# Performance work log

Hardware: AMD Instinct MI355X
Metric: run time of the kernel (lower is better)

Reference implementation:

```python
import jax, jax.numpy as jnp
import numpy as np

HEADS = 16
D_MODEL = 1024
D_K = D_MODEL // HEADS
BATCH = 4
SEQ = 1024
NEG_BIG = -1000000000.0


def setup_inputs() -> dict:
    key = jax.random.key(0)
    ks = jax.random.split(key, 7)
    s = 1.0 / np.sqrt(D_MODEL)
    return {
        "q": jax.random.normal(ks[0], (BATCH, SEQ, D_MODEL), jnp.float32),
        "k": jax.random.normal(ks[1], (BATCH, SEQ, D_MODEL), jnp.float32),
        "v": jax.random.normal(ks[2], (BATCH, SEQ, D_MODEL), jnp.float32),
        "Wq": jax.random.normal(ks[3], (D_MODEL, D_MODEL), jnp.float32) * s,
        "Wk": jax.random.normal(ks[4], (D_MODEL, D_MODEL), jnp.float32) * s,
        "Wv": jax.random.normal(ks[5], (D_MODEL, D_MODEL), jnp.float32) * s,
        "Wo": jax.random.normal(ks[6], (D_MODEL, D_MODEL), jnp.float32) * s,
    }


def reference(q, k, v, Wq, Wk, Wv, Wo):
    bs = q.shape[0]
    residual = q
    # torch Linear(bias=False): x @ W.T ; then the module's quirky reshape
    # view(bs, h, -1, d_k) on the contiguous [bs, seq, d_model] buffer.
    qh = (q @ Wq.T).reshape(bs, HEADS, -1, D_K)   # [b, h, s, d_k]
    kh = (k @ Wk.T).reshape(bs, HEADS, -1, D_K)
    vh = (v @ Wv.T).reshape(bs, HEADS, -1, D_K)
    scores = jnp.einsum("bhqd,bhkd->bhqk", qh, kh) / jnp.sqrt(
        jnp.asarray(D_K, qh.dtype))
    # data-dependent mask: exact-zero scores get -1e9 before softmax
    scores = jnp.where(scores == 0, jnp.asarray(NEG_BIG, scores.dtype), scores)
    attn = jax.nn.softmax(scores, axis=-1)  # dropout is identity in eval mode
    out = jnp.einsum("bhqk,bhkd->bhqd", attn, vh)  # [b, h, s, d_k]
    concat = jnp.swapaxes(out, 1, 2).reshape(bs, -1, D_MODEL)
    return concat @ Wo.T + residual
```

## Files before the change

### kernel.cpp

```cpp
#include <hip/hip_runtime.h>
#include <stdint.h>

typedef __bf16 bf16x8 __attribute__((ext_vector_type(8)));
typedef __bf16 bf16x2v __attribute__((ext_vector_type(2)));
typedef float f32x4 __attribute__((ext_vector_type(4)));
typedef uint16_t u16x8 __attribute__((ext_vector_type(8)));
typedef uint16_t u16x4 __attribute__((ext_vector_type(4)));

#define DMODEL 1024
#define K1SC 0.1803368801111244f

__device__ __forceinline__ uint16_t bfc(float f) {
  __bf16 h = (__bf16)f;
  return __builtin_bit_cast(uint16_t, h);
}
__device__ __forceinline__ uint32_t pk32(float a, float b) {
  bf16x2v t = {(__bf16)a, (__bf16)b};
  return __builtin_bit_cast(uint32_t, t);
}
__device__ __forceinline__ void gld16(const void* src, void* dst) {
  __builtin_amdgcn_global_load_lds((const __attribute__((address_space(1))) void*)src,
                                   (__attribute__((address_space(3))) void*)dst, 16, 0, 0);
}

__global__ void cvt_all_kernel(const float* __restrict__ q, const float* __restrict__ k,
                               const float* __restrict__ v, const float* __restrict__ Wq,
                               const float* __restrict__ Wk, const float* __restrict__ Wv,
                               const float* __restrict__ Wo, uint16_t* __restrict__ qb,
                               uint16_t* __restrict__ kb, uint16_t* __restrict__ vb,
                               uint16_t* __restrict__ Wqb, uint16_t* __restrict__ Wkb,
                               uint16_t* __restrict__ Wvb, uint16_t* __restrict__ Wob) {
  int bid = blockIdx.x;
  const float* src;
  uint16_t* dst;
  int off;
  if (bid < 12288) {
    int s = bid >> 12;
    src = s == 0 ? q : (s == 1 ? k : v);
    dst = s == 0 ? qb : (s == 1 ? kb : vb);
    off = bid & 4095;
  } else {
    int r = bid - 12288;
    int s = r >> 10;
    src = s == 0 ? Wq : (s == 1 ? Wk : (s == 2 ? Wv : Wo));
    dst = s == 0 ? Wqb : (s == 1 ? Wkb : (s == 2 ? Wvb : Wob));
    off = r & 1023;
  }
  int i = off * 256 + threadIdx.x;
  f32x4 x = ((const f32x4*)src)[i];
  u16x4 r;
#pragma unroll
  for (int j = 0; j < 4; ++j) r[j] = bfc(x[j]);
  ((u16x4*)dst)[i] = r;
}

__global__ __launch_bounds__(256, 2)
void gemm_qkv_kernel(const uint16_t* __restrict__ A0, const uint16_t* __restrict__ A1,
                     const uint16_t* __restrict__ A2, const uint16_t* __restrict__ W0,
                     const uint16_t* __restrict__ W1, const uint16_t* __restrict__ W2,
                     uint16_t* __restrict__ C0, uint16_t* __restrict__ C1,
                     uint16_t* __restrict__ C2) {
  int orig = blockIdx.x;
  int lin = (orig & 7) * 96 + (orig >> 3);
  int z = lin >> 8;
  int rem = lin & 255;
  int m0 = (rem >> 3) * 128, n0 = (rem & 7) * 128;

  const uint16_t* A = z == 0 ? A0 : (z == 1 ? A1 : A2);
  const uint16_t* Bw = z == 0 ? W0 : (z == 1 ? W1 : W2);
  uint16_t* C = z == 0 ? C0 : (z == 1 ? C1 : C2);
  const float osc = (z == 0) ? K1SC : 1.0f;

  __shared__ __align__(16) uint16_t As[2][128 * 32];
  __shared__ __align__(16) uint16_t Bs[2][128 * 32];
  const int t = threadIdx.x;
  const int lane = t & 63;
  const int w = t >> 6;
  const int wr = w >> 1, wc = w & 1;
  const int lr = lane & 15, ksl = lane >> 4;
  const int sw2 = (lr & 3) << 4;

  f32x4 acc[4][4];
#pragma unroll
  for (int m = 0; m < 4; ++m)
#pragma unroll
    for (int n = 0; n < 4; ++n) acc[m][n] = (f32x4){0.f, 0.f, 0.f, 0.f};

  auto stage = [&](int buf, int k0) {
#pragma unroll
    for (int cc = 0; cc < 2; ++cc) {
      int idx = cc * 256 + t;
      int row = idx >> 2, ch = idx & 3;
      int so = ((ch * 16) ^ ((row & 3) << 4)) >> 1;
      gld16(A + (size_t)(m0 + row) * DMODEL + k0 + so, &As[buf][idx * 8]);
    }
#pragma unroll
    for (int cc = 0; cc < 2; ++cc) {
      int idx = cc * 256 + t;
      int row = idx >> 2, ch = idx & 3;
      int so = ((ch * 16) ^ ((row & 3) << 4)) >> 1;
      gld16(Bw + (size_t)(n0 + row) * DMODEL + k0 + so, &Bs[buf][idx * 8]);
    }
  };

  stage(0, 0);
  __syncthreads();

  int cur = 0;
#pragma unroll 1
  for (int kt = 0; kt < 32; ++kt) {
    if (kt < 31) stage(cur ^ 1, (kt + 1) * 32);
    const char* Ab = (const char*)&As[cur][0];
    const char* Bb = (const char*)&Bs[cur][0];
    const int co = (ksl * 16) ^ sw2;
    bf16x8 af[4], bfv[4];
#pragma unroll
    for (int m = 0; m < 4; ++m)
      af[m] = *(const bf16x8*)(Ab + (wr * 64 + m * 16 + lr) * 64 + co);
#pragma unroll
    for (int n = 0; n < 4; ++n)
      bfv[n] = *(const bf16x8*)(Bb + (wc * 64 + n * 16 + lr) * 64 + co);
    __builtin_amdgcn_s_setprio(1);
#pragma unroll
    for (int m = 0; m < 4; ++m)
#pragma unroll
      for (int n = 0; n < 4; ++n)
        acc[m][n] = __builtin_amdgcn_mfma_f32_16x16x32_bf16(af[m], bfv[n], acc[m][n], 0, 0, 0);
    __builtin_amdgcn_s_setprio(0);
    __syncthreads();
    cur ^= 1;
  }

#pragma unroll
  for (int m = 0; m < 4; ++m) {
#pragma unroll
    for (int n = 0; n < 4; ++n) {
      int col = n0 + wc * 64 + n * 16 + lr;
#pragma unroll
      for (int r = 0; r < 4; ++r) {
        int row = m0 + wr * 64 + m * 16 + ksl * 4 + r;
        C[(size_t)row * DMODEL + col] = bfc(acc[m][n][r] * osc);
      }
    }
  }
}

__global__ __launch_bounds__(256, 2)
void gemm_o_kernel(const uint16_t* __restrict__ A, const uint16_t* __restrict__ Bw,
                   float* __restrict__ Cf, const float* __restrict__ resid) {
  int orig = blockIdx.x;
  int lin = (orig & 7) * 64 + (orig >> 3);
  int m0 = (lin >> 3) * 64, n0 = (lin & 7) * 128;

  __shared__ __align__(16) uint16_t As[2][64 * 32];
  __shared__ __align__(16) uint16_t Bs[2][128 * 32];
  const int t = threadIdx.x;
  const int lane = t & 63;
  const int w = t >> 6;
  const int wr = w >> 1, wc = w & 1;
  const int lr = lane & 15, ksl = lane >> 4;
  const int sw2 = (lr & 3) << 4;

  f32x4 acc[2][4];
#pragma unroll
  for (int m = 0; m < 2; ++m)
#pragma unroll
    for (int n = 0; n < 4; ++n) acc[m][n] = (f32x4){0.f, 0.f, 0.f, 0.f};

  auto stage = [&](int buf, int k0) {
    {
      int row = t >> 2, ch = t & 3;
      int so = ((ch * 16) ^ ((row & 3) << 4)) >> 1;
      gld16(A + (size_t)(m0 + row) * DMODEL + k0 + so, &As[buf][t * 8]);
    }
#pragma unroll
    for (int cc = 0; cc < 2; ++cc) {
      int idx = cc * 256 + t;
      int row = idx >> 2, ch = idx & 3;
      int so = ((ch * 16) ^ ((row & 3) << 4)) >> 1;
      gld16(Bw + (size_t)(n0 + row) * DMODEL + k0 + so, &Bs[buf][idx * 8]);
    }
  };

  stage(0, 0);
  __syncthreads();

  int cur = 0;
#pragma unroll 1
  for (int kt = 0; kt < 32; ++kt) {
    if (kt < 31) stage(cur ^ 1, (kt + 1) * 32);
    const char* Ab = (const char*)&As[cur][0];
    const char* Bb = (const char*)&Bs[cur][0];
    const int co = (ksl * 16) ^ sw2;
    bf16x8 af[2], bfv[4];
#pragma unroll
    for (int m = 0; m < 2; ++m)
      af[m] = *(const bf16x8*)(Ab + (wr * 32 + m * 16 + lr) * 64 + co);
#pragma unroll
    for (int n = 0; n < 4; ++n)
      bfv[n] = *(const bf16x8*)(Bb + (wc * 64 + n * 16 + lr) * 64 + co);
    __builtin_amdgcn_s_setprio(1);
#pragma unroll
    for (int m = 0; m < 2; ++m)
#pragma unroll
      for (int n = 0; n < 4; ++n)
        acc[m][n] = __builtin_amdgcn_mfma_f32_16x16x32_bf16(af[m], bfv[n], acc[m][n], 0, 0, 0);
    __builtin_amdgcn_s_setprio(0);
    __syncthreads();
    cur ^= 1;
  }

#pragma unroll
  for (int m = 0; m < 2; ++m) {
#pragma unroll
    for (int n = 0; n < 4; ++n) {
      int col = n0 + wc * 64 + n * 16 + lr;
#pragma unroll
      for (int r = 0; r < 4; ++r) {
        int row = m0 + wr * 32 + m * 16 + ksl * 4 + r;
        size_t idx = (size_t)row * DMODEL + col;
        Cf[idx] = acc[m][n][r] + resid[idx];
      }
    }
  }
}

__global__ __launch_bounds__(256, 2)
void attn_mfma_kernel(const uint16_t* __restrict__ Pq, const uint16_t* __restrict__ Pk,
                      const uint16_t* __restrict__ Pv, uint16_t* __restrict__ Cc) {
  __shared__ __align__(16) uint16_t Ks[2][64 * 64];
  __shared__ __align__(16) uint16_t Vts[2][64 * 64];
  __shared__ __align__(16) uint16_t Ps[4][16 * 64];

  const int t = threadIdx.x;
  const int w = t >> 6;
  const int lane = t & 63;
  const int lr = lane & 15;
  const int ksl = lane >> 4;
  int orig = blockIdx.x;
  int lin = (orig & 7) * 128 + (orig >> 3);
  const int bh = lin >> 4, qt = lin & 15;
  const int b = bh >> 4, h = bh & 15;

  const uint16_t* Qb = Pq + (size_t)bh * 65536 + (size_t)qt * 64 * 64;
  const uint16_t* Kb = Pk + (size_t)bh * 65536;
  const uint16_t* Vb = Pv + (size_t)bh * 65536;

  bf16x8 qf[2];
  {
    const uint16_t* qrow = Qb + (size_t)(w * 16 + lr) * 64 + ksl * 8;
    qf[0] = *(const bf16x8*)(qrow);
    qf[1] = *(const bf16x8*)(qrow + 32);
  }

  f32x4 Oa[4];
#pragma unroll
  for (int n = 0; n < 4; ++n) Oa[n] = (f32x4){0.f, 0.f, 0.f, 0.f};
  f32x4 lsum4 = {0.f, 0.f, 0.f, 0.f};

  const int p2 = t & 31;
  const int c8 = t >> 5;
  const int sw = (lr & 7) << 4;
  u16x8 va, vb2;

  auto stageK = [&](int buf, int kt) {
#pragma unroll
    for (int cc = 0; cc < 2; ++cc) {
      int idx = cc * 256 + t;
      int row = idx >> 3;
      int bo = (idx & 7) * 16;
      int srcb = bo ^ ((row & 7) << 4);
      gld16(Kb + (size_t)(kt * 64 + row) * 64 + (srcb >> 1), &Ks[buf][idx * 8]);
    }
  };
  auto loadV = [&](int kt) {
    const uint16_t* s0 = Vb + (size_t)(kt * 64 + p2 * 2) * 64 + c8 * 8;
    va = *(const u16x8*)s0;
    vb2 = *(const u16x8*)(s0 + 64);
  };
  auto writeV = [&](int buf) {
    char* base = (char*)&Vts[buf][0];
#pragma unroll
    for (int i = 0; i < 8; ++i) {
      int d = c8 * 8 + i;
      uint32_t val = (uint32_t)va[i] | ((uint32_t)vb2[i] << 16);
      *(uint32_t*)(base + d * 128 + ((p2 * 4) ^ ((d & 7) << 4))) = val;
    }
  };

  stageK(0, 0);
  loadV(0);
  writeV(0);
  __syncthreads();

  int cur = 0;
#pragma unroll 1
  for (int kt = 0; kt < 16; ++kt) {
    if (kt < 15) { stageK(cur ^ 1, kt + 1); loadV(kt + 1); }

    f32x4 S[4];
#pragma unroll
    for (int n = 0; n < 4; ++n) S[n] = (f32x4){0.f, 0.f, 0.f, 0.f};
    __builtin_amdgcn_s_setprio(1);
#pragma unroll
    for (int n = 0; n < 4; ++n) {
      const char* kbp = (const char*)&Ks[cur][0] + (n * 16 + lr) * 128;
#pragma unroll
      for (int c = 0; c < 2; ++c) {
        bf16x8 kf = *(const bf16x8*)(kbp + ((c * 64 + ksl * 16) ^ sw));
        S[n] = __builtin_amdgcn_mfma_f32_16x16x32_bf16(kf, qf[c], S[n], 0, 0, 0);
      }
    }
    __builtin_amdgcn_s_setprio(0);

    f32x4 psum = {0.f, 0.f, 0.f, 0.f};
    f32x4 p4[4];
#pragma unroll
    for (int n = 0; n < 4; ++n) {
#pragma unroll
      for (int r = 0; r < 4; ++r) {
        float x = S[n][r];
        float e = __builtin_amdgcn_exp2f(x);
        p4[n][r] = (x == 0.f) ? 0.f : e;
      }
      psum += p4[n];
    }
    lsum4 += psum;

    char* pb = (char*)&Ps[w][0] + lr * 128;
#pragma unroll
    for (int n = 0; n < 4; ++n) {
      int co = (n * 16 + ksl * 4) * 2;
      *(uint32_t*)(pb + (co ^ sw)) = pk32(p4[n][0], p4[n][1]);
      *(uint32_t*)(pb + ((co + 4) ^ sw)) = pk32(p4[n][2], p4[n][3]);
    }

    __builtin_amdgcn_s_setprio(1);
#pragma unroll
    for (int c = 0; c < 2; ++c) {
      bf16x8 pf = *(const bf16x8*)(pb + ((c * 64 + ksl * 16) ^ sw));
#pragma unroll
      for (int n = 0; n < 4; ++n) {
        const char* vbp = (const char*)&Vts[cur][0] + (n * 16 + lr) * 128;
        bf16x8 vf = *(const bf16x8*)(vbp + ((c * 64 + ksl * 16) ^ sw));
        Oa[n] = __builtin_amdgcn_mfma_f32_16x16x32_bf16(pf, vf, Oa[n], 0, 0, 0);
      }
    }
    __builtin_amdgcn_s_setprio(0);

    if (kt < 15) writeV(cur ^ 1);
    __syncthreads();
    cur ^= 1;
  }

  float lrow = (lsum4[0] + lsum4[1]) + (lsum4[2] + lsum4[3]);
  lrow += __shfl_xor(lrow, 16);
  lrow += __shfl_xor(lrow, 32);
  f32x4 inv4;
#pragma unroll
  for (int r = 0; r < 4; ++r) inv4[r] = 1.f / __shfl(lrow, ksl * 4 + r);

  uint16_t* dst = Cc + (size_t)b * 1048576 + (size_t)(qt * 64 + w * 16) * 1024 + h * 64;
#pragma unroll
  for (int r = 0; r < 4; ++r) {
    int qq = ksl * 4 + r;
#pragma unroll
    for (int n = 0; n < 4; ++n) {
      dst[qq * 1024 + n * 16 + lr] = bfc(Oa[n][r] * inv4[r]);
    }
  }
}

extern "C" void kernel_launch(void* const* d_in, const int* in_sizes, int n_in,
                              void* d_out, int out_size, void* d_ws, size_t ws_size,
                              hipStream_t stream) {
  const float* q  = (const float*)d_in[0];
  const float* k  = (const float*)d_in[1];
  const float* v  = (const float*)d_in[2];
  const float* Wq = (const float*)d_in[3];
  const float* Wk = (const float*)d_in[4];
  const float* Wv = (const float*)d_in[5];
  const float* Wo = (const float*)d_in[6];
  float* out = (float*)d_out;
  char* ws = (char*)d_ws;
  const size_t MB = 1u << 20;
  uint16_t* qb  = (uint16_t*)(ws + 0 * MB);
  uint16_t* kb  = (uint16_t*)(ws + 8 * MB);
  uint16_t* vb  = (uint16_t*)(ws + 16 * MB);
  uint16_t* Wqb = (uint16_t*)(ws + 24 * MB);
  uint16_t* Wkb = (uint16_t*)(ws + 26 * MB);
  uint16_t* Wvb = (uint16_t*)(ws + 28 * MB);
  uint16_t* Wob = (uint16_t*)(ws + 30 * MB);
  uint16_t* Pq  = (uint16_t*)(ws + 32 * MB);
  uint16_t* Pk  = (uint16_t*)(ws + 40 * MB);
  uint16_t* Pv  = (uint16_t*)(ws + 48 * MB);
  uint16_t* Cc  = (uint16_t*)(ws + 56 * MB);

  cvt_all_kernel<<<16384, 256, 0, stream>>>(q, k, v, Wq, Wk, Wv, Wo,
                                            qb, kb, vb, Wqb, Wkb, Wvb, Wob);

  gemm_qkv_kernel<<<768, 256, 0, stream>>>(qb, kb, vb, Wqb, Wkb, Wvb,
                                           Pq, Pk, Pv);

  attn_mfma_kernel<<<1024, 256, 0, stream>>>(Pq, Pk, Pv, Cc);

  gemm_o_kernel<<<512, 256, 0, stream>>>(Cc, Wob, out, q);
}
```

Baseline: 107.1 us.

## Pre-transpose V and feed P directly from registers via 16x16x16 MFMA

Adds a separate kernel that transposes the V projection per head into a d-major buffer, reusing the qb workspace, so the attention kernel can stage V with async global-to-LDS loads instead of register loads and scattered LDS writes. When the 16x16x16 bf16 MFMA builtin is available, P is taken straight from the score accumulators as the A operand, which removes the per-wave P round trip through LDS. Occupancy hint raised to 4 blocks per SM. Costs an extra kernel launch and an additional V read/write through global memory.

```diff
diff --git a/kernel.cpp b/kernel.cpp
--- a/kernel.cpp
+++ b/kernel.cpp
@@ -6,9 +6,17 @@
 typedef float f32x4 __attribute__((ext_vector_type(4)));
 typedef uint16_t u16x8 __attribute__((ext_vector_type(8)));
 typedef uint16_t u16x4 __attribute__((ext_vector_type(4)));
+typedef uint32_t u32x2 __attribute__((ext_vector_type(2)));
+typedef short s16x4 __attribute__((ext_vector_type(4)));
 
 #define DMODEL 1024
 #define K1SC 0.1803368801111244f
+
+#if __has_builtin(__builtin_amdgcn_mfma_f32_16x16x16bf16_1k)
+#define HAS_MFMA16 1
+#else
+#define HAS_MFMA16 0
+#endif
 
 __device__ __forceinline__ uint16_t bfc(float f) {
   __bf16 h = (__bf16)f;
@@ -145,6 +153,32 @@
   }
 }
 
+__global__ void transposeV_kernel(const uint16_t* __restrict__ Pv,
+                                  uint16_t* __restrict__ Vt) {
+  __shared__ uint16_t Ts[64 * 65];
+  const int bh = blockIdx.x >> 4, kt = blockIdx.x & 15;
+  const uint16_t* src = Pv + (size_t)bh * 65536 + (size_t)kt * 64 * 64;
+  uint16_t* dst = Vt + (size_t)bh * 65536 + kt * 64;
+  const int t = threadIdx.x;
+#pragma unroll
+  for (int p = 0; p < 2; ++p) {
+    int idx = p * 256 + t;
+    int kr = idx >> 3, c8 = (idx & 7) * 8;
+    u16x8 ld = *(const u16x8*)(src + kr * 64 + c8);
+#pragma unroll
+    for (int i = 0; i < 8; ++i) Ts[kr * 65 + c8 + i] = ld[i];
+  }
+  __syncthreads();
+  const int dk = t >> 2, jg = t & 3;
+  u16x8 o0, o1;
+#pragma unroll
+  for (int jj = 0; jj < 8; ++jj) o0[jj] = Ts[(jg * 16 + jj) * 65 + dk];
+#pragma unroll
+  for (int jj = 0; jj < 8; ++jj) o1[jj] = Ts[(jg * 16 + 8 + jj) * 65 + dk];
+  *(u16x8*)(dst + (size_t)dk * 1024 + jg * 16) = o0;
+  *(u16x8*)(dst + (size_t)dk * 1024 + jg * 16 + 8) = o1;
+}
+
 __global__ __launch_bounds__(256, 2)
 void gemm_o_kernel(const uint16_t* __restrict__ A, const uint16_t* __restrict__ Bw,
                    float* __restrict__ Cf, const float* __restrict__ resid) {
@@ -225,12 +259,14 @@
   }
 }
 
-__global__ __launch_bounds__(256, 2)
+__global__ __launch_bounds__(256, 4)
 void attn_mfma_kernel(const uint16_t* __restrict__ Pq, const uint16_t* __restrict__ Pk,
-                      const uint16_t* __restrict__ Pv, uint16_t* __restrict__ Cc) {
+                      const uint16_t* __restrict__ Vt, uint16_t* __restrict__ Cc) {
   __shared__ __align__(16) uint16_t Ks[2][64 * 64];
   __shared__ __align__(16) uint16_t Vts[2][64 * 64];
+#if !HAS_MFMA16
   __shared__ __align__(16) uint16_t Ps[4][16 * 64];
+#endif
 
   const int t = threadIdx.x;
   const int w = t >> 6;
@@ -244,7 +280,7 @@
 
   const uint16_t* Qb = Pq + (size_t)bh * 65536 + (size_t)qt * 64 * 64;
   const uint16_t* Kb = Pk + (size_t)bh * 65536;
-  const uint16_t* Vb = Pv + (size_t)bh * 65536;
+  const uint16_t* Vb = Vt + (size_t)bh * 65536;
 
   bf16x8 qf[2];
   {
@@ -258,10 +294,7 @@
   for (int n = 0; n < 4; ++n) Oa[n] = (f32x4){0.f, 0.f, 0.f, 0.f};
   f32x4 lsum4 = {0.f, 0.f, 0.f, 0.f};
 
-  const int p2 = t & 31;
-  const int c8 = t >> 5;
   const int sw = (lr & 7) << 4;
-  u16x8 va, vb2;
 
   auto stageK = [&](int buf, int kt) {
 #pragma unroll
@@ -273,30 +306,25 @@
       gld16(Kb + (size_t)(kt * 64 + row) * 64 + (srcb >> 1), &Ks[buf][idx * 8]);
     }
   };
-  auto loadV = [&](int kt) {
-    const uint16_t* s0 = Vb + (size_t)(kt * 64 + p2 * 2) * 64 + c8 * 8;
-    va = *(const u16x8*)s0;
-    vb2 = *(const u16x8*)(s0 + 64);
+  auto stageV = [&](int buf, int kt) {
+#pragma unroll
+    for (int cc = 0; cc < 2; ++cc) {
+      int idx = cc * 256 + t;
+      int row = idx >> 3;
+      int bo = (idx & 7) * 16;
+      int srcb = bo ^ ((row & 7) << 4);
+      gld16(Vb + (size_t)row * 1024 + kt * 64 + (srcb >> 1), &Vts[buf][idx * 8]);
+    }
   };
-  auto writeV = [&](int buf) {
-    char* base = (char*)&Vts[buf][0];
-#pragma unroll
-    for (int i = 0; i < 8; ++i) {
-      int d = c8 * 8 + i;
-      uint32_t val = (uint32_t)va[i] | ((uint32_t)vb2[i] << 16);
-      *(uint32_t*)(base + d * 128 + ((p2 * 4) ^ ((d & 7) << 4))) = val;
-    }
-  };
 
   stageK(0, 0);
-  loadV(0);
-  writeV(0);
+  stageV(0, 0);
   __syncthreads();
 
   int cur = 0;
 #pragma unroll 1
   for (int kt = 0; kt < 16; ++kt) {
-    if (kt < 15) { stageK(cur ^ 1, kt + 1); loadV(kt + 1); }
+    if (kt < 15) { stageK(cur ^ 1, kt + 1); stageV(cur ^ 1, kt + 1); }
 
     f32x4 S[4];
 #pragma unroll
@@ -327,6 +355,21 @@
     }
     lsum4 += psum;
 
+#if HAS_MFMA16
+    const char* vbase = (const char*)&Vts[cur][0];
+    __builtin_amdgcn_s_setprio(1);
+#pragma unroll
+    for (int n = 0; n < 4; ++n) {
+      u32x2 pa32 = {pk32(p4[n][0], p4[n][1]), pk32(p4[n][2], p4[n][3])};
+      s16x4 pa = __builtin_bit_cast(s16x4, pa32);
+#pragma unroll
+      for (int nd = 0; nd < 4; ++nd) {
+        s16x4 vf = *(const s16x4*)(vbase + (nd * 16 + lr) * 128 + ((n * 32 + ksl * 8) ^ sw));
+        Oa[nd] = __builtin_amdgcn_mfma_f32_16x16x16bf16_1k(pa, vf, Oa[nd], 0, 0, 0);
+      }
+    }
+    __builtin_amdgcn_s_setprio(0);
+#else
     char* pb = (char*)&Ps[w][0] + lr * 128;
 #pragma unroll
     for (int n = 0; n < 4; ++n) {
@@ -334,7 +377,6 @@
       *(uint32_t*)(pb + (co ^ sw)) = pk32(p4[n][0], p4[n][1]);
       *(uint32_t*)(pb + ((co + 4) ^ sw)) = pk32(p4[n][2], p4[n][3]);
     }
-
     __builtin_amdgcn_s_setprio(1);
 #pragma unroll
     for (int c = 0; c < 2; ++c) {
@@ -347,8 +389,8 @@
       }
     }
     __builtin_amdgcn_s_setprio(0);
-
-    if (kt < 15) writeV(cur ^ 1);
+#endif
+
     __syncthreads();
     cur ^= 1;
   }
@@ -395,6 +437,7 @@
   uint16_t* Pk  = (uint16_t*)(ws + 40 * MB);
   uint16_t* Pv  = (uint16_t*)(ws + 48 * MB);
   uint16_t* Cc  = (uint16_t*)(ws + 56 * MB);
+  uint16_t* Vtb = (uint16_t*)(ws + 0 * MB);
 
   cvt_all_kernel<<<16384, 256, 0, stream>>>(q, k, v, Wq, Wk, Wv, Wo,
                                             qb, kb, vb, Wqb, Wkb, Wvb, Wob);
@@ -402,7 +445,9 @@
   gemm_qkv_kernel<<<768, 256, 0, stream>>>(qb, kb, vb, Wqb, Wkb, Wvb,
                                            Pq, Pk, Pv);
 
-  attn_mfma_kernel<<<1024, 256, 0, stream>>>(Pq, Pk, Pv, Cc);
+  transposeV_kernel<<<1024, 256, 0, stream>>>(Pv, Vtb);
+
+  attn_mfma_kernel<<<1024, 256, 0, stream>>>(Pq, Pk, Vtb, Cc);
 
   gemm_o_kernel<<<512, 256, 0, stream>>>(Cc, Wob, out, q);
 }
```

New measurement: 110.8 us. 3.4% more time.

## Fuse fp32-to-bf16 conversion into GEMM staging and keep P in registers

Applied to the files above, without the earlier changes.

Drops the separate conversion kernel. The QKV and output GEMMs now load fp32 inputs and weights through registers, convert them to bf16, and store them into padded shared memory, which saves a full pass over the inputs and one launch. The attention kernel stops round-tripping P through shared memory and feeds packed registers directly into 16x16x16 MFMAs, with LDS offsets precomputed. Occupancy hints are raised. In exchange the GEMMs lose async global-to-LDS loads, use more registers, and read twice the global bytes of the bf16 inputs.

```diff
diff --git a/kernel.cpp b/kernel.cpp
--- a/kernel.cpp
+++ b/kernel.cpp
@@ -5,7 +5,8 @@
 typedef __bf16 bf16x2v __attribute__((ext_vector_type(2)));
 typedef float f32x4 __attribute__((ext_vector_type(4)));
 typedef uint16_t u16x8 __attribute__((ext_vector_type(8)));
-typedef uint16_t u16x4 __attribute__((ext_vector_type(4)));
+typedef uint32_t u32x2 __attribute__((ext_vector_type(2)));
+typedef short s16x4 __attribute__((ext_vector_type(4)));
 
 #define DMODEL 1024
 #define K1SC 0.1803368801111244f
@@ -23,62 +24,56 @@
                                    (__attribute__((address_space(3))) void*)dst, 16, 0, 0);
 }
 
-__global__ void cvt_all_kernel(const float* __restrict__ q, const float* __restrict__ k,
-                               const float* __restrict__ v, const float* __restrict__ Wq,
-                               const float* __restrict__ Wk, const float* __restrict__ Wv,
-                               const float* __restrict__ Wo, uint16_t* __restrict__ qb,
-                               uint16_t* __restrict__ kb, uint16_t* __restrict__ vb,
-                               uint16_t* __restrict__ Wqb, uint16_t* __restrict__ Wkb,
-                               uint16_t* __restrict__ Wvb, uint16_t* __restrict__ Wob) {
-  int bid = blockIdx.x;
-  const float* src;
-  uint16_t* dst;
-  int off;
-  if (bid < 12288) {
-    int s = bid >> 12;
-    src = s == 0 ? q : (s == 1 ? k : v);
-    dst = s == 0 ? qb : (s == 1 ? kb : vb);
-    off = bid & 4095;
-  } else {
-    int r = bid - 12288;
-    int s = r >> 10;
-    src = s == 0 ? Wq : (s == 1 ? Wk : (s == 2 ? Wv : Wo));
-    dst = s == 0 ? Wqb : (s == 1 ? Wkb : (s == 2 ? Wvb : Wob));
-    off = r & 1023;
-  }
-  int i = off * 256 + threadIdx.x;
-  f32x4 x = ((const f32x4*)src)[i];
-  u16x4 r;
-#pragma unroll
-  for (int j = 0; j < 4; ++j) r[j] = bfc(x[j]);
-  ((u16x4*)dst)[i] = r;
-}
-
-__global__ __launch_bounds__(256, 2)
-void gemm_qkv_kernel(const uint16_t* __restrict__ A0, const uint16_t* __restrict__ A1,
-                     const uint16_t* __restrict__ A2, const uint16_t* __restrict__ W0,
-                     const uint16_t* __restrict__ W1, const uint16_t* __restrict__ W2,
+__global__ __launch_bounds__(256, 3)
+void gemm_qkv_kernel(const float* __restrict__ A0, const float* __restrict__ A1,
+                     const float* __restrict__ A2, const float* __restrict__ W0,
+                     const float* __restrict__ W1, const float* __restrict__ W2,
                      uint16_t* __restrict__ C0, uint16_t* __restrict__ C1,
                      uint16_t* __restrict__ C2) {
   int orig = blockIdx.x;
   int lin = (orig & 7) * 96 + (orig >> 3);
-  int z = lin >> 8;
-  int rem = lin & 255;
+  int z = lin >> 8, rem = lin & 255;
   int m0 = (rem >> 3) * 128, n0 = (rem & 7) * 128;
 
-  const uint16_t* A = z == 0 ? A0 : (z == 1 ? A1 : A2);
-  const uint16_t* Bw = z == 0 ? W0 : (z == 1 ? W1 : W2);
+  const float* A  = z == 0 ? A0 : (z == 1 ? A1 : A2);
+  const float* Bw = z == 0 ? W0 : (z == 1 ? W1 : W2);
   uint16_t* C = z == 0 ? C0 : (z == 1 ? C1 : C2);
   const float osc = (z == 0) ? K1SC : 1.0f;
 
-  __shared__ __align__(16) uint16_t As[2][128 * 32];
-  __shared__ __align__(16) uint16_t Bs[2][128 * 32];
+  __shared__ __align__(16) char As[2][128 * 80];
+  __shared__ __align__(16) char Bs[2][128 * 80];
   const int t = threadIdx.x;
   const int lane = t & 63;
   const int w = t >> 6;
   const int wr = w >> 1, wc = w & 1;
   const int lr = lane & 15, ksl = lane >> 4;
-  const int sw2 = (lr & 3) << 4;
+
+  const int srow = t >> 2, sch = t & 3;
+  const float* pa = A + (size_t)(m0 + srow) * DMODEL + sch * 8;
+  const float* pb = Bw + (size_t)(n0 + srow) * DMODEL + sch * 8;
+  const int sd = srow * 80 + sch * 16;
+
+  f32x4 la0, la1, la2, la3, lb0, lb1, lb2, lb3;
+  auto LOAD = [&]() {
+    la0 = *(const f32x4*)pa;           la1 = *(const f32x4*)(pa + 4);
+    la2 = *(const f32x4*)(pa + 65536); la3 = *(const f32x4*)(pa + 65540);
+    lb0 = *(const f32x4*)pb;           lb1 = *(const f32x4*)(pb + 4);
+    lb2 = *(const f32x4*)(pb + 65536); lb3 = *(const f32x4*)(pb + 65540);
+  };
+  auto pack2 = [](f32x4 x, f32x4 y) {
+    u16x8 r;
+#pragma unroll
+    for (int j = 0; j < 4; ++j) { r[j] = bfc(x[j]); r[4 + j] = bfc(y[j]); }
+    return r;
+  };
+  auto STORE = [&](int buf) {
+    char* ab = &As[buf][0];
+    char* bb = &Bs[buf][0];
+    *(u16x8*)(ab + sd) = pack2(la0, la1);
+    *(u16x8*)(ab + sd + 5120) = pack2(la2, la3);
+    *(u16x8*)(bb + sd) = pack2(lb0, lb1);
+    *(u16x8*)(bb + sd + 5120) = pack2(lb2, lb3);
+  };
 
   f32x4 acc[4][4];
 #pragma unroll
@@ -86,40 +81,23 @@
 #pragma unroll
     for (int n = 0; n < 4; ++n) acc[m][n] = (f32x4){0.f, 0.f, 0.f, 0.f};
 
-  auto stage = [&](int buf, int k0) {
-#pragma unroll
-    for (int cc = 0; cc < 2; ++cc) {
-      int idx = cc * 256 + t;
-      int row = idx >> 2, ch = idx & 3;
-      int so = ((ch * 16) ^ ((row & 3) << 4)) >> 1;
-      gld16(A + (size_t)(m0 + row) * DMODEL + k0 + so, &As[buf][idx * 8]);
-    }
-#pragma unroll
-    for (int cc = 0; cc < 2; ++cc) {
-      int idx = cc * 256 + t;
-      int row = idx >> 2, ch = idx & 3;
-      int so = ((ch * 16) ^ ((row & 3) << 4)) >> 1;
-      gld16(Bw + (size_t)(n0 + row) * DMODEL + k0 + so, &Bs[buf][idx * 8]);
-    }
-  };
-
-  stage(0, 0);
+  LOAD();
+  STORE(0);
   __syncthreads();
 
   int cur = 0;
 #pragma unroll 1
   for (int kt = 0; kt < 32; ++kt) {
-    if (kt < 31) stage(cur ^ 1, (kt + 1) * 32);
-    const char* Ab = (const char*)&As[cur][0];
-    const char* Bb = (const char*)&Bs[cur][0];
-    const int co = (ksl * 16) ^ sw2;
+    if (kt < 31) { pa += 32; pb += 32; LOAD(); }
+    const char* Ab = &As[cur][0];
+    const char* Bb = &Bs[cur][0];
     bf16x8 af[4], bfv[4];
 #pragma unroll
     for (int m = 0; m < 4; ++m)
-      af[m] = *(const bf16x8*)(Ab + (wr * 64 + m * 16 + lr) * 64 + co);
+      af[m] = *(const bf16x8*)(Ab + (wr * 64 + m * 16 + lr) * 80 + ksl * 16);
 #pragma unroll
     for (int n = 0; n < 4; ++n)
-      bfv[n] = *(const bf16x8*)(Bb + (wc * 64 + n * 16 + lr) * 64 + co);
+      bfv[n] = *(const bf16x8*)(Bb + (wc * 64 + n * 16 + lr) * 80 + ksl * 16);
     __builtin_amdgcn_s_setprio(1);
 #pragma unroll
     for (int m = 0; m < 4; ++m)
@@ -127,6 +105,7 @@
       for (int n = 0; n < 4; ++n)
         acc[m][n] = __builtin_amdgcn_mfma_f32_16x16x32_bf16(af[m], bfv[n], acc[m][n], 0, 0, 0);
     __builtin_amdgcn_s_setprio(0);
+    if (kt < 31) STORE(cur ^ 1);
     __syncthreads();
     cur ^= 1;
   }
@@ -145,21 +124,45 @@
   }
 }
 
-__global__ __launch_bounds__(256, 2)
-void gemm_o_kernel(const uint16_t* __restrict__ A, const uint16_t* __restrict__ Bw,
+__global__ __launch_bounds__(256, 4)
+void gemm_o_kernel(const uint16_t* __restrict__ Ac, const float* __restrict__ Bw,
                    float* __restrict__ Cf, const float* __restrict__ resid) {
   int orig = blockIdx.x;
   int lin = (orig & 7) * 64 + (orig >> 3);
   int m0 = (lin >> 3) * 64, n0 = (lin & 7) * 128;
 
-  __shared__ __align__(16) uint16_t As[2][64 * 32];
-  __shared__ __align__(16) uint16_t Bs[2][128 * 32];
+  __shared__ __align__(16) char As[2][64 * 80];
+  __shared__ __align__(16) char Bs[2][128 * 80];
   const int t = threadIdx.x;
   const int lane = t & 63;
   const int w = t >> 6;
   const int wr = w >> 1, wc = w & 1;
   const int lr = lane & 15, ksl = lane >> 4;
-  const int sw2 = (lr & 3) << 4;
+
+  const int srow = t >> 2, sch = t & 3;
+  const uint16_t* pc = Ac + (size_t)(m0 + srow) * DMODEL + sch * 8;
+  const float* pb = Bw + (size_t)(n0 + srow) * DMODEL + sch * 8;
+  const int sd = srow * 80 + sch * 16;
+
+  u16x8 lc;
+  f32x4 lb0, lb1, lb2, lb3;
+  auto LOAD = [&]() {
+    lc = *(const u16x8*)pc;
+    lb0 = *(const f32x4*)pb;           lb1 = *(const f32x4*)(pb + 4);
+    lb2 = *(const f32x4*)(pb + 65536); lb3 = *(const f32x4*)(pb + 65540);
+  };
+  auto pack2 = [](f32x4 x, f32x4 y) {
+    u16x8 r;
+#pragma unroll
+    for (int j = 0; j < 4; ++j) { r[j] = bfc(x[j]); r[4 + j] = bfc(y[j]); }
+    return r;
+  };
+  auto STORE = [&](int buf) {
+    *(u16x8*)(&As[buf][0] + sd) = lc;
+    char* bb = &Bs[buf][0];
+    *(u16x8*)(bb + sd) = pack2(lb0, lb1);
+    *(u16x8*)(bb + sd + 5120) = pack2(lb2, lb3);
+  };
 
   f32x4 acc[2][4];
 #pragma unroll
@@ -167,38 +170,23 @@
 #pragma unroll
     for (int n = 0; n < 4; ++n) acc[m][n] = (f32x4){0.f, 0.f, 0.f, 0.f};
 
-  auto stage = [&](int buf, int k0) {
-    {
-      int row = t >> 2, ch = t & 3;
-      int so = ((ch * 16) ^ ((row & 3) << 4)) >> 1;
-      gld16(A + (size_t)(m0 + row) * DMODEL + k0 + so, &As[buf][t * 8]);
-    }
-#pragma unroll
-    for (int cc = 0; cc < 2; ++cc) {
-      int idx = cc * 256 + t;
-      int row = idx >> 2, ch = idx & 3;
-      int so = ((ch * 16) ^ ((row & 3) << 4)) >> 1;
-      gld16(Bw + (size_t)(n0 + row) * DMODEL + k0 + so, &Bs[buf][idx * 8]);
-    }
-  };
-
-  stage(0, 0);
+  LOAD();
+  STORE(0);
   __syncthreads();
 
   int cur = 0;
 #pragma unroll 1
   for (int kt = 0; kt < 32; ++kt) {
-    if (kt < 31) stage(cur ^ 1, (kt + 1) * 32);
-    const char* Ab = (const char*)&As[cur][0];
-    const char* Bb = (const char*)&Bs[cur][0];
-    const int co = (ksl * 16) ^ sw2;
+    if (kt < 31) { pc += 32; pb += 32; LOAD(); }
+    const char* Ab = &As[cur][0];
+    const char* Bb = &Bs[cur][0];
     bf16x8 af[2], bfv[4];
 #pragma unroll
     for (int m = 0; m < 2; ++m)
-      af[m] = *(const bf16x8*)(Ab + (wr * 32 + m * 16 + lr) * 64 + co);
+      af[m] = *(const bf16x8*)(Ab + (wr * 32 + m * 16 + lr) * 80 + ksl * 16);
 #pragma unroll
     for (int n = 0; n < 4; ++n)
-      bfv[n] = *(const bf16x8*)(Bb + (wc * 64 + n * 16 + lr) * 64 + co);
+      bfv[n] = *(const bf16x8*)(Bb + (wc * 64 + n * 16 + lr) * 80 + ksl * 16);
     __builtin_amdgcn_s_setprio(1);
 #pragma unroll
     for (int m = 0; m < 2; ++m)
@@ -206,6 +194,7 @@
       for (int n = 0; n < 4; ++n)
         acc[m][n] = __builtin_amdgcn_mfma_f32_16x16x32_bf16(af[m], bfv[n], acc[m][n], 0, 0, 0);
     __builtin_amdgcn_s_setprio(0);
+    if (kt < 31) STORE(cur ^ 1);
     __syncthreads();
     cur ^= 1;
   }
@@ -225,12 +214,11 @@
   }
 }
 
-__global__ __launch_bounds__(256, 2)
+__global__ __launch_bounds__(256, 4)
 void attn_mfma_kernel(const uint16_t* __restrict__ Pq, const uint16_t* __restrict__ Pk,
                       const uint16_t* __restrict__ Pv, uint16_t* __restrict__ Cc) {
   __shared__ __align__(16) uint16_t Ks[2][64 * 64];
   __shared__ __align__(16) uint16_t Vts[2][64 * 64];
-  __shared__ __align__(16) uint16_t Ps[4][16 * 64];
 
   const int t = threadIdx.x;
   const int w = t >> 6;
@@ -242,15 +230,15 @@
   const int bh = lin >> 4, qt = lin & 15;
   const int b = bh >> 4, h = bh & 15;
 
-  const uint16_t* Qb = Pq + (size_t)bh * 65536 + (size_t)qt * 64 * 64;
+  const uint16_t* Qb = Pq + (size_t)bh * 65536 + (size_t)qt * 4096;
   const uint16_t* Kb = Pk + (size_t)bh * 65536;
   const uint16_t* Vb = Pv + (size_t)bh * 65536;
 
-  bf16x8 qf[2];
+  bf16x8 qf0, qf1;
   {
     const uint16_t* qrow = Qb + (size_t)(w * 16 + lr) * 64 + ksl * 8;
-    qf[0] = *(const bf16x8*)(qrow);
-    qf[1] = *(const bf16x8*)(qrow + 32);
+    qf0 = *(const bf16x8*)(qrow);
+    qf1 = *(const bf16x8*)(qrow + 32);
   }
 
   f32x4 Oa[4];
@@ -258,45 +246,63 @@
   for (int n = 0; n < 4; ++n) Oa[n] = (f32x4){0.f, 0.f, 0.f, 0.f};
   f32x4 lsum4 = {0.f, 0.f, 0.f, 0.f};
 
+  const int sw = (lr & 7) << 4;
   const int p2 = t & 31;
   const int c8 = t >> 5;
-  const int sw = (lr & 7) << 4;
+
+  int qko[4][2], pvo[4][4], wvo[8];
+#pragma unroll
+  for (int n = 0; n < 4; ++n) {
+#pragma unroll
+    for (int c = 0; c < 2; ++c) qko[n][c] = (n * 16 + lr) * 128 + ((c * 64 + ksl * 16) ^ sw);
+#pragma unroll
+    for (int nd = 0; nd < 4; ++nd) pvo[n][nd] = (nd * 16 + lr) * 128 + ((n * 32 + ksl * 8) ^ sw);
+  }
+#pragma unroll
+  for (int i = 0; i < 8; ++i) {
+    int d = c8 * 8 + i;
+    wvo[i] = d * 128 + ((p2 * 4) ^ ((d & 7) << 4));
+  }
+
+  const int sr0 = t >> 3;
+  const int sc0 = (((t & 7) * 16) ^ ((sr0 & 7) << 4)) >> 1;
+  const uint16_t* srcK = Kb + (size_t)sr0 * 64 + sc0;
+  const uint16_t* srcV = Vb + (size_t)(p2 * 2) * 64 + c8 * 8;
+  const int kd0 = t * 16, kd1 = (256 + t) * 16;
+
+  char* kb0 = (char*)&Ks[0][0];
+  char* kb1 = (char*)&Ks[1][0];
+  char* vb0 = (char*)&Vts[0][0];
+  char* vb1 = (char*)&Vts[1][0];
+
   u16x8 va, vb2;
-
-  auto stageK = [&](int buf, int kt) {
-#pragma unroll
-    for (int cc = 0; cc < 2; ++cc) {
-      int idx = cc * 256 + t;
-      int row = idx >> 3;
-      int bo = (idx & 7) * 16;
-      int srcb = bo ^ ((row & 7) << 4);
-      gld16(Kb + (size_t)(kt * 64 + row) * 64 + (srcb >> 1), &Ks[buf][idx * 8]);
-    }
-  };
-  auto loadV = [&](int kt) {
-    const uint16_t* s0 = Vb + (size_t)(kt * 64 + p2 * 2) * 64 + c8 * 8;
-    va = *(const u16x8*)s0;
-    vb2 = *(const u16x8*)(s0 + 64);
-  };
-  auto writeV = [&](int buf) {
-    char* base = (char*)&Vts[buf][0];
+  auto stageK = [&](char* kbuf) {
+    gld16(srcK, kbuf + kd0);
+    gld16(srcK + 2048, kbuf + kd1);
+  };
+  auto loadV = [&]() {
+    va = *(const u16x8*)srcV;
+    vb2 = *(const u16x8*)(srcV + 64);
+  };
+  auto writeV = [&](char* vbuf) {
 #pragma unroll
     for (int i = 0; i < 8; ++i) {
-      int d = c8 * 8 + i;
       uint32_t val = (uint32_t)va[i] | ((uint32_t)vb2[i] << 16);
-      *(uint32_t*)(base + d * 128 + ((p2 * 4) ^ ((d & 7) << 4))) = val;
-    }
-  };
-
-  stageK(0, 0);
-  loadV(0);
-  writeV(0);
+      *(uint32_t*)(vbuf + wvo[i]) = val;
+    }
+  };
+
+  stageK(kb0);
+  loadV();
+  writeV(vb0);
   __syncthreads();
 
-  int cur = 0;
+  const char* kcur = kb0; char* knx = kb1;
+  const char* vcur = vb0; char* vnx = vb1;
+
 #pragma unroll 1
   for (int kt = 0; kt < 16; ++kt) {
-    if (kt < 15) { stageK(cur ^ 1, kt + 1); loadV(kt + 1); }
+    if (kt < 15) { srcK += 4096; stageK(knx); srcV += 4096; loadV(); }
 
     f32x4 S[4];
 #pragma unroll
@@ -304,12 +310,10 @@
     __builtin_amdgcn_s_setprio(1);
 #pragma unroll
     for (int n = 0; n < 4; ++n) {
-      const char* kbp = (const char*)&Ks[cur][0] + (n * 16 + lr) * 128;
-#pragma unroll
-      for (int c = 0; c < 2; ++c) {
-        bf16x8 kf = *(const bf16x8*)(kbp + ((c * 64 + ksl * 16) ^ sw));
-        S[n] = __builtin_amdgcn_mfma_f32_16x16x32_bf16(kf, qf[c], S[n], 0, 0, 0);
-      }
+      bf16x8 kf0 = *(const bf16x8*)(kcur + qko[n][0]);
+      bf16x8 kf1 = *(const bf16x8*)(kcur + qko[n][1]);
+      S[n] = __builtin_amdgcn_mfma_f32_16x16x32_bf16(kf0, qf0, S[n], 0, 0, 0);
+      S[n] = __builtin_amdgcn_mfma_f32_16x16x32_bf16(kf1, qf1, S[n], 0, 0, 0);
     }
     __builtin_amdgcn_s_setprio(0);
 
@@ -327,30 +331,23 @@
     }
     lsum4 += psum;
 
-    char* pb = (char*)&Ps[w][0] + lr * 128;
-#pragma unroll
-    for (int n = 0; n < 4; ++n) {
-      int co = (n * 16 + ksl * 4) * 2;
-      *(uint32_t*)(pb + (co ^ sw)) = pk32(p4[n][0], p4[n][1]);
-      *(uint32_t*)(pb + ((co + 4) ^ sw)) = pk32(p4[n][2], p4[n][3]);
-    }
-
     __builtin_amdgcn_s_setprio(1);
 #pragma unroll
-    for (int c = 0; c < 2; ++c) {
-      bf16x8 pf = *(const bf16x8*)(pb + ((c * 64 + ksl * 16) ^ sw));
-#pragma unroll
-      for (int n = 0; n < 4; ++n) {
-        const char* vbp = (const char*)&Vts[cur][0] + (n * 16 + lr) * 128;
-        bf16x8 vf = *(const bf16x8*)(vbp + ((c * 64 + ksl * 16) ^ sw));
-        Oa[n] = __builtin_amdgcn_mfma_f32_16x16x32_bf16(pf, vf, Oa[n], 0, 0, 0);
+    for (int n = 0; n < 4; ++n) {
+      u32x2 pa32 = {pk32(p4[n][0], p4[n][1]), pk32(p4[n][2], p4[n][3])};
+      s16x4 pa = __builtin_bit_cast(s16x4, pa32);
+#pragma unroll
+      for (int nd = 0; nd < 4; ++nd) {
+        s16x4 vf = *(const s16x4*)(vcur + pvo[n][nd]);
+        Oa[nd] = __builtin_amdgcn_mfma_f32_16x16x16bf16_1k(pa, vf, Oa[nd], 0, 0, 0);
       }
     }
     __builtin_amdgcn_s_setprio(0);
 
-    if (kt < 15) writeV(cur ^ 1);
+    if (kt < 15) writeV(vnx);
     __syncthreads();
-    cur ^= 1;
+    const char* tk = kcur; kcur = knx; knx = (char*)tk;
+    const char* tv = vcur; vcur = vnx; vnx = (char*)tv;
   }
 
   float lrow = (lsum4[0] + lsum4[1]) + (lsum4[2] + lsum4[3]);
@@ -384,25 +381,14 @@
   float* out = (float*)d_out;
   char* ws = (char*)d_ws;
   const size_t MB = 1u << 20;
-  uint16_t* qb  = (uint16_t*)(ws + 0 * MB);
-  uint16_t* kb  = (uint16_t*)(ws + 8 * MB);
-  uint16_t* vb  = (uint16_t*)(ws + 16 * MB);
-  uint16_t* Wqb = (uint16_t*)(ws + 24 * MB);
-  uint16_t* Wkb = (uint16_t*)(ws + 26 * MB);
-  uint16_t* Wvb = (uint16_t*)(ws + 28 * MB);
-  uint16_t* Wob = (uint16_t*)(ws + 30 * MB);
-  uint16_t* Pq  = (uint16_t*)(ws + 32 * MB);
-  uint16_t* Pk  = (uint16_t*)(ws + 40 * MB);
-  uint16_t* Pv  = (uint16_t*)(ws + 48 * MB);
-  uint16_t* Cc  = (uint16_t*)(ws + 56 * MB);
-
-  cvt_all_kernel<<<16384, 256, 0, stream>>>(q, k, v, Wq, Wk, Wv, Wo,
-                                            qb, kb, vb, Wqb, Wkb, Wvb, Wob);
-
-  gemm_qkv_kernel<<<768, 256, 0, stream>>>(qb, kb, vb, Wqb, Wkb, Wvb,
-                                           Pq, Pk, Pv);
+  uint16_t* Pq = (uint16_t*)(ws + 0 * MB);
+  uint16_t* Pk = (uint16_t*)(ws + 8 * MB);
+  uint16_t* Pv = (uint16_t*)(ws + 16 * MB);
+  uint16_t* Cc = (uint16_t*)(ws + 24 * MB);
+
+  gemm_qkv_kernel<<<768, 256, 0, stream>>>(q, k, v, Wq, Wk, Wv, Pq, Pk, Pv);
 
   attn_mfma_kernel<<<1024, 256, 0, stream>>>(Pq, Pk, Pv, Cc);
 
-  gemm_o_kernel<<<512, 256, 0, stream>>>(Cc, Wob, out, q);
-}
+  gemm_o_kernel<<<512, 256, 0, stream>>>(Cc, Wo, out, q);
+}
```

After: 101.0 us. 1.06x faster.

## Feed softmax probabilities to PV MFMA directly from registers, dropping LDS round trip

Applied to the files above, without the earlier changes.

The attention kernel no longer writes P to shared memory and reads it back. Instead the S accumulator layout is reused directly as the A operand of 16x16x16 bf16 MFMAs, with V fragments read at matching offsets. LDS offsets are precomputed, buffers are swapped by pointer, and launch bounds are raised to 4 blocks per CU for occupancy. The trade-off is twice as many smaller MFMAs for PV and tighter register limits that could cause spills.

```diff
diff --git a/kernel.cpp b/kernel.cpp
--- a/kernel.cpp
+++ b/kernel.cpp
@@ -6,6 +6,8 @@
 typedef float f32x4 __attribute__((ext_vector_type(4)));
 typedef uint16_t u16x8 __attribute__((ext_vector_type(8)));
 typedef uint16_t u16x4 __attribute__((ext_vector_type(4)));
+typedef uint32_t u32x2 __attribute__((ext_vector_type(2)));
+typedef short s16x4 __attribute__((ext_vector_type(4)));
 
 #define DMODEL 1024
 #define K1SC 0.1803368801111244f
@@ -225,12 +227,11 @@
   }
 }
 
-__global__ __launch_bounds__(256, 2)
+__global__ __launch_bounds__(256, 4)
 void attn_mfma_kernel(const uint16_t* __restrict__ Pq, const uint16_t* __restrict__ Pk,
                       const uint16_t* __restrict__ Pv, uint16_t* __restrict__ Cc) {
   __shared__ __align__(16) uint16_t Ks[2][64 * 64];
   __shared__ __align__(16) uint16_t Vts[2][64 * 64];
-  __shared__ __align__(16) uint16_t Ps[4][16 * 64];
 
   const int t = threadIdx.x;
   const int w = t >> 6;
@@ -242,15 +243,15 @@
   const int bh = lin >> 4, qt = lin & 15;
   const int b = bh >> 4, h = bh & 15;
 
-  const uint16_t* Qb = Pq + (size_t)bh * 65536 + (size_t)qt * 64 * 64;
+  const uint16_t* Qb = Pq + (size_t)bh * 65536 + (size_t)qt * 4096;
   const uint16_t* Kb = Pk + (size_t)bh * 65536;
   const uint16_t* Vb = Pv + (size_t)bh * 65536;
 
-  bf16x8 qf[2];
+  bf16x8 qf0, qf1;
   {
     const uint16_t* qrow = Qb + (size_t)(w * 16 + lr) * 64 + ksl * 8;
-    qf[0] = *(const bf16x8*)(qrow);
-    qf[1] = *(const bf16x8*)(qrow + 32);
+    qf0 = *(const bf16x8*)(qrow);
+    qf1 = *(const bf16x8*)(qrow + 32);
   }
 
   f32x4 Oa[4];
@@ -258,45 +259,63 @@
   for (int n = 0; n < 4; ++n) Oa[n] = (f32x4){0.f, 0.f, 0.f, 0.f};
   f32x4 lsum4 = {0.f, 0.f, 0.f, 0.f};
 
+  const int sw = (lr & 7) << 4;
   const int p2 = t & 31;
   const int c8 = t >> 5;
-  const int sw = (lr & 7) << 4;
+
+  int qko[4][2], pvo[4][4], wvo[8];
+#pragma unroll
+  for (int n = 0; n < 4; ++n) {
+#pragma unroll
+    for (int c = 0; c < 2; ++c) qko[n][c] = (n * 16 + lr) * 128 + ((c * 64 + ksl * 16) ^ sw);
+#pragma unroll
+    for (int nd = 0; nd < 4; ++nd) pvo[n][nd] = (nd * 16 + lr) * 128 + ((n * 32 + ksl * 8) ^ sw);
+  }
+#pragma unroll
+  for (int i = 0; i < 8; ++i) {
+    int d = c8 * 8 + i;
+    wvo[i] = d * 128 + ((p2 * 4) ^ ((d & 7) << 4));
+  }
+
+  const int sr0 = t >> 3;
+  const int sc0 = (((t & 7) * 16) ^ ((sr0 & 7) << 4)) >> 1;
+  const uint16_t* srcK = Kb + (size_t)sr0 * 64 + sc0;
+  const uint16_t* srcV = Vb + (size_t)(p2 * 2) * 64 + c8 * 8;
+  const int kd0 = t * 16, kd1 = (256 + t) * 16;
+
+  char* kb0 = (char*)&Ks[0][0];
+  char* kb1 = (char*)&Ks[1][0];
+  char* vb0 = (char*)&Vts[0][0];
+  char* vb1 = (char*)&Vts[1][0];
+
   u16x8 va, vb2;
-
-  auto stageK = [&](int buf, int kt) {
-#pragma unroll
-    for (int cc = 0; cc < 2; ++cc) {
-      int idx = cc * 256 + t;
-      int row = idx >> 3;
-      int bo = (idx & 7) * 16;
-      int srcb = bo ^ ((row & 7) << 4);
-      gld16(Kb + (size_t)(kt * 64 + row) * 64 + (srcb >> 1), &Ks[buf][idx * 8]);
-    }
+  auto stageK = [&](char* kbuf) {
+    gld16(srcK, kbuf + kd0);
+    gld16(srcK + 2048, kbuf + kd1);
   };
-  auto loadV = [&](int kt) {
-    const uint16_t* s0 = Vb + (size_t)(kt * 64 + p2 * 2) * 64 + c8 * 8;
-    va = *(const u16x8*)s0;
-    vb2 = *(const u16x8*)(s0 + 64);
+  auto loadV = [&]() {
+    va = *(const u16x8*)srcV;
+    vb2 = *(const u16x8*)(srcV + 64);
   };
-  auto writeV = [&](int buf) {
-    char* base = (char*)&Vts[buf][0];
+  auto writeV = [&](char* vbuf) {
 #pragma unroll
     for (int i = 0; i < 8; ++i) {
-      int d = c8 * 8 + i;
       uint32_t val = (uint32_t)va[i] | ((uint32_t)vb2[i] << 16);
-      *(uint32_t*)(base + d * 128 + ((p2 * 4) ^ ((d & 7) << 4))) = val;
+      *(uint32_t*)(vbuf + wvo[i]) = val;
     }
   };
 
-  stageK(0, 0);
-  loadV(0);
-  writeV(0);
+  stageK(kb0);
+  loadV();
+  writeV(vb0);
   __syncthreads();
 
-  int cur = 0;
+  const char* kcur = kb0; char* knx = kb1;
+  const char* vcur = vb0; char* vnx = vb1;
+
 #pragma unroll 1
   for (int kt = 0; kt < 16; ++kt) {
-    if (kt < 15) { stageK(cur ^ 1, kt + 1); loadV(kt + 1); }
+    if (kt < 15) { srcK += 4096; stageK(knx); srcV += 4096; loadV(); }
 
     f32x4 S[4];
 #pragma unroll
@@ -304,12 +323,10 @@
     __builtin_amdgcn_s_setprio(1);
 #pragma unroll
     for (int n = 0; n < 4; ++n) {
-      const char* kbp = (const char*)&Ks[cur][0] + (n * 16 + lr) * 128;
-#pragma unroll
-      for (int c = 0; c < 2; ++c) {
-        bf16x8 kf = *(const bf16x8*)(kbp + ((c * 64 + ksl * 16) ^ sw));
-        S[n] = __builtin_amdgcn_mfma_f32_16x16x32_bf16(kf, qf[c], S[n], 0, 0, 0);
-      }
+      bf16x8 kf0 = *(const bf16x8*)(kcur + qko[n][0]);
+      bf16x8 kf1 = *(const bf16x8*)(kcur + qko[n][1]);
+      S[n] = __builtin_amdgcn_mfma_f32_16x16x32_bf16(kf0, qf0, S[n], 0, 0, 0);
+      S[n] = __builtin_amdgcn_mfma_f32_16x16x32_bf16(kf1, qf1, S[n], 0, 0, 0);
     }
     __builtin_amdgcn_s_setprio(0);
 
@@ -327,30 +344,23 @@
     }
     lsum4 += psum;
 
-    char* pb = (char*)&Ps[w][0] + lr * 128;
-#pragma unroll
-    for (int n = 0; n < 4; ++n) {
-      int co = (n * 16 + ksl * 4) * 2;
-      *(uint32_t*)(pb + (co ^ sw)) = pk32(p4[n][0], p4[n][1]);
-      *(uint32_t*)(pb + ((co + 4) ^ sw)) = pk32(p4[n][2], p4[n][3]);
-    }
-
     __builtin_amdgcn_s_setprio(1);
 #pragma unroll
-    for (int c = 0; c < 2; ++c) {
-      bf16x8 pf = *(const bf16x8*)(pb + ((c * 64 + ksl * 16) ^ sw));
-#pragma unroll
-      for (int n = 0; n < 4; ++n) {
-        const char* vbp = (const char*)&Vts[cur][0] + (n * 16 + lr) * 128;
-        bf16x8 vf = *(const bf16x8*)(vbp + ((c * 64 + ksl * 16) ^ sw));
-        Oa[n] = __builtin_amdgcn_mfma_f32_16x16x32_bf16(pf, vf, Oa[n], 0, 0, 0);
+    for (int n = 0; n < 4; ++n) {
+      u32x2 pa32 = {pk32(p4[n][0], p4[n][1]), pk32(p4[n][2], p4[n][3])};
+      s16x4 pa = __builtin_bit_cast(s16x4, pa32);
+#pragma unroll
+      for (int nd = 0; nd < 4; ++nd) {
+        s16x4 vf = *(const s16x4*)(vcur + pvo[n][nd]);
+        Oa[nd] = __builtin_amdgcn_mfma_f32_16x16x16bf16_1k(pa, vf, Oa[nd], 0, 0, 0);
       }
     }
     __builtin_amdgcn_s_setprio(0);
 
-    if (kt < 15) writeV(cur ^ 1);
+    if (kt < 15) writeV(vnx);
     __syncthreads();
-    cur ^= 1;
+    const char* tk = kcur; kcur = knx; knx = (char*)tk;
+    const char* tv = vcur; vcur = vnx; vnx = (char*)tv;
   }
 
   float lrow = (lsum4[0] + lsum4[1]) + (lsum4[2] + lsum4[3]);
```

Result: no change. 105.2 us (-1.8%).
